# Kernel optimization log

Hardware: AMD Instinct MI355X
Metric: run time of the kernel (lower is better)

The kernel has to match this reference:

```python
import jax, jax.numpy as jnp
import numpy as np
from jax import lax

SEQ_LEN = 64
BATCH = 256
NUM_TAG = 32
EMBED = 256
HIDDEN = 256


def gru_cell(x, h, W_ih, W_hh, b_ih, b_hh):
    # PyTorch GRU cell: gates ordered (r, z, n)
    gi = x @ W_ih.T + b_ih
    gh = h @ W_hh.T + b_hh
    ir, iz, i_n = jnp.split(gi, 3, axis=-1)
    hr, hz, h_n = jnp.split(gh, 3, axis=-1)
    r = jax.nn.sigmoid(ir + hr)
    z = jax.nn.sigmoid(iz + hz)
    n = jnp.tanh(i_n + r * h_n)
    return (1.0 - z) * n + z * h


def setup_inputs() -> dict:
    key = jax.random.key(0)
    ks = jax.random.split(key, 9)
    emissions = jax.random.normal(ks[0], (SEQ_LEN, BATCH, NUM_TAG), jnp.float32)
    tags = jax.random.randint(ks[1], (SEQ_LEN, BATCH), 0, NUM_TAG)
    mask = jnp.ones((SEQ_LEN, BATCH), jnp.float32)
    s = float(1.0 / np.sqrt(HIDDEN))
    embedding = jax.random.normal(ks[2], (NUM_TAG + 1, EMBED), jnp.float32) * 0.1
    W_ih = jax.random.normal(ks[3], (3 * HIDDEN, EMBED), jnp.float32) * s
    W_hh = jax.random.normal(ks[4], (3 * HIDDEN, HIDDEN), jnp.float32) * s
    b_ih = jax.random.normal(ks[5], (3 * HIDDEN,), jnp.float32) * s
    b_hh = jax.random.normal(ks[6], (3 * HIDDEN,), jnp.float32) * s
    W_lin = jax.random.normal(ks[7], (NUM_TAG, HIDDEN), jnp.float32) * s
    b_lin = jnp.zeros((NUM_TAG,), jnp.float32)
    return {"emissions": emissions, "tags": tags, "mask": mask,
            "embedding": embedding, "W_ih": W_ih, "W_hh": W_hh,
            "b_ih": b_ih, "b_hh": b_hh, "W_lin": W_lin, "b_lin": b_lin}


def reference(emissions, tags, mask, embedding, W_ih, W_hh, b_ih, b_hh, W_lin, b_lin):
    L, B, T = emissions.shape
    H = W_hh.shape[1]
    K = T  # self.topk = num_tag in the original module
    mask = mask.astype(emissions.dtype)
    gru = lambda x, h: gru_cell(x, h, W_ih, W_hh, b_ih, b_hh)
    lin = lambda h: h @ W_lin.T + b_lin

    # shared initial step with start symbol y0 = num_tag
    x0 = jnp.broadcast_to(embedding[T], (B, embedding.shape[1]))
    h0 = jnp.zeros((B, H), emissions.dtype)
    h1 = gru(x0, h0)                      # (B,H)
    trans0 = lin(h1)                      # (B,T)
    em0 = emissions[0]
    bidx = jnp.arange(B)

    # ---- path score (faithful: emissions[0] gathered at EVERY timestep) ----
    t0 = tags[0]
    ps0 = (trans0[bidx, t0] + em0[bidx, t0]) * mask[0]

    def ps_step(carry, xs):
        h, s = carry
        pre, cur, m = xs
        h = gru(embedding[pre], h)
        tr = lin(h)
        s = s + (tr[bidx, cur] + em0[bidx, cur]) * m
        return (h, s), None

    (_, path_score), _ = lax.scan(ps_step, (h1, ps0), (tags[:-1], tags[1:], mask[1:]))

    # ---- approximate log-partition via beam search with K = num_tag beams ----
    s_init = (trans0 + em0) * mask[0][:, None]
    scores, beam_tags = lax.top_k(s_init, K)          # (B,K), tag-id indices
    hidden = jnp.broadcast_to(h1[:, None, :], (B, K, H))

    def lp_step(carry, xs):
        scores, beam_tags, hidden = carry
        em_t, m_t = xs
        x = embedding[beam_tags]                                  # (B,K,E)
        hnew = gru(x.reshape(B * K, -1), hidden.reshape(B * K, H)).reshape(B, K, H)
        tr = lin(hnew)                                            # (B,K,T)
        # faithful quirk: prior beam scores gathered by previous TAG id (K == T)
        base = jnp.take_along_axis(scores, beam_tags, axis=1)[:, :, None]
        cand = base + (tr + em_t[:, None, :]) * m_t[:, None, None]  # (B,K,T)
        new_scores, idx = lax.top_k(cand.reshape(B, K * T), K)
        new_tags = idx % T
        parent = idx // T
        new_hidden = jnp.take_along_axis(hnew, parent[:, :, None], axis=1)
        return (new_scores, new_tags, new_hidden), None

    (scores, _, _), _ = lax.scan(lp_step, (scores, beam_tags, hidden),
                                 (emissions[1:], mask[1:]))

    log_z = jax.nn.logsumexp(scores, axis=1)
    return (path_score - log_z).sum()
```

## Files before the change

### kernel.cpp

```cpp
#include <hip/hip_runtime.h>

#define SEQ 64
#define BAT 256
#define NT 32
#define EMB 256
#define HID 256
#define G3 768

typedef __bf16 bf16x8 __attribute__((ext_vector_type(8)));
typedef __bf16 bf16x4 __attribute__((ext_vector_type(4)));
typedef float f32x4 __attribute__((ext_vector_type(4)));
typedef unsigned long long ulx2 __attribute__((ext_vector_type(2)));

#define GL2S 265
#define HQS  280

__device__ __forceinline__ float sigm_fast(float x) {
    return __builtin_amdgcn_rcpf(1.f + __expf(-x));
}
__device__ __forceinline__ float tanh_fast(float x) {
    return 1.f - 2.f * __builtin_amdgcn_rcpf(__expf(2.f * x) + 1.f);
}
__device__ __forceinline__ float sigm(float x) {
    x = fminf(fmaxf(x, -30.f), 30.f);
    return 1.f / (1.f + __expf(-x));
}
__device__ __forceinline__ float tanhr(float x) {
    x = fminf(fmaxf(x, -15.f), 15.f);
    float e = __expf(2.f * x);
    return (e - 1.f) / (e + 1.f);
}

__global__ void k_pre(const float* __restrict__ emb, const float* __restrict__ W_ih,
                      const float* __restrict__ b_ih, const float* __restrict__ W_hh,
                      const float* __restrict__ W_lin, const float* __restrict__ b_hh,
                      const float* __restrict__ b_lin,
                      float* __restrict__ G, int2* __restrict__ Wpk8, __bf16* __restrict__ Wlpk,
                      float* __restrict__ h1, float* __restrict__ tr0)
{
    const int tid = threadIdx.x;
    const int blk = blockIdx.x;
    if (blk < 33) {
        __shared__ float es[EMB];
        __shared__ float hs[HID];
        es[tid] = emb[blk * EMB + tid];
        __syncthreads();
        const float4* e4 = (const float4*)es;
        float gv[3];
        #pragma unroll
        for (int g = 0; g < 3; ++g) {
            int c = g * HID + tid;
            const float4* w4 = (const float4*)(W_ih + c * EMB);
            float acc = b_ih[c];
            #pragma unroll 8
            for (int i = 0; i < EMB / 4; ++i) {
                float4 a = e4[i], w = w4[i];
                acc += a.x * w.x + a.y * w.y + a.z * w.z + a.w * w.w;
            }
            G[blk * G3 + c] = acc;
            gv[g] = acc;
        }
        if (blk == 32) {
            float r = sigm(gv[0] + b_hh[tid]);
            float z = sigm(gv[1] + b_hh[HID + tid]);
            float n = tanhr(gv[2] + r * b_hh[2 * HID + tid]);
            float h = (1.f - z) * n;
            h1[tid] = h; hs[tid] = h;
            __syncthreads();
            if (tid < NT) {
                const float4* w4 = (const float4*)(W_lin + tid * HID);
                const float4* h4 = (const float4*)hs;
                float acc = b_lin[tid];
                #pragma unroll 8
                for (int i = 0; i < HID / 4; ++i) {
                    float4 a = h4[i], w = w4[i];
                    acc += a.x * w.x + a.y * w.y + a.z * w.z + a.w * w.w;
                }
                tr0[tid] = acc;
            }
        }
    } else if (blk < 129) {
        int idx  = (blk - 33) * 256 + tid;
        int c    = idx >> 9;
        int rem  = idx & 511;
        int kt   = rem >> 6;
        int lane = rem & 63;
        int row  = c * 16 + (lane & 15);
        int col  = kt * 32 + (lane >> 4) * 8;
        const float* src = W_hh + row * 256 + col;
        int lo = __builtin_amdgcn_cvt_pk_fp8_f32(src[0], src[1], 0, 0);
        lo     = __builtin_amdgcn_cvt_pk_fp8_f32(src[2], src[3], lo, 1);
        int hi = __builtin_amdgcn_cvt_pk_fp8_f32(src[4], src[5], 0, 0);
        hi     = __builtin_amdgcn_cvt_pk_fp8_f32(src[6], src[7], hi, 1);
        Wpk8[idx] = make_int2(lo, hi);
    } else {
        int i2   = (blk - 129) * 256 + tid;
        int nt   = i2 >> 9;
        int rem  = i2 & 511;
        int kt   = rem >> 6;
        int lane = rem & 63;
        int row  = nt * 16 + (lane & 15);
        int col  = kt * 32 + (lane >> 4) * 8;
        const float* src = W_lin + row * 256 + col;
        bf16x8 v;
        #pragma unroll
        for (int j = 0; j < 8; ++j) v[j] = (__bf16)src[j];
        *(bf16x8*)(Wlpk + i2 * 8) = v;
    }
}

#define CLEANK32(mk, l32)                                          \
    _Pragma("unroll")                                              \
    for (int off_ = 16; off_ >= 1; off_ >>= 1) {                   \
        unsigned long long o_ = __shfl_xor((mk), off_, 64);        \
        bool up_ = ((l32) & off_) == 0;                            \
        if (up_ == (o_ > (mk))) (mk) = o_;                         \
    }

__global__ __launch_bounds__(1024, 1) void k_main(
    const float* __restrict__ em, const int* __restrict__ tags, const float* __restrict__ mask,
    const float* __restrict__ G, const float* __restrict__ h1w, const float* __restrict__ tr0w,
    const long* __restrict__ Wpk8, const __bf16* __restrict__ Wlpk,
    const float* __restrict__ bhhg, const float* __restrict__ bling,
    float* __restrict__ out)
{
    __shared__ __attribute__((aligned(16))) __bf16 gl2[33 * GL2S * 4];
    __shared__ __attribute__((aligned(16))) __bf16 hbuf[2][33 * 264];
    __shared__ __attribute__((aligned(16))) unsigned char hqb[2][33 * HQS];
    __shared__ __attribute__((aligned(16))) __bf16 wlin[8192];
    __shared__ __attribute__((aligned(16))) unsigned long long candk[32 * 34];
    __shared__ __attribute__((aligned(16))) unsigned long long srtk[16 * 33];
    __shared__ float trs32[33];
    __shared__ float em_s[SEQ * NT];
    __shared__ float mask_s[SEQ];
    __shared__ int tags_s[SEQ];
    __shared__ float scores[NT];
    __shared__ int par[NT];
    __shared__ int parbt[NT];
    __shared__ float s_ps;

    const int tid = threadIdx.x;
    const int b = blockIdx.x;
    const int w = tid >> 6;
    const int lane = tid & 63;
    const int q = lane >> 4;
    const int l15 = lane & 15;
    const int j = w * 16 + l15;

    long wreg[24];
    #pragma unroll
    for (int g = 0; g < 3; ++g)
        #pragma unroll
        for (int kt = 0; kt < 8; ++kt)
            wreg[g * 8 + kt] = Wpk8[((g * 16 + w) * 8 + kt) * 64 + lane];
    const float br_ = bhhg[j], bz_ = bhhg[256 + j], bn_ = bhhg[512 + j];
    float bl_ = 0.f;
    if (w < 6) bl_ = bling[(w & 1) * 16 + l15];

    if (tid < 64) mask_s[tid] = mask[tid * BAT + b];
    else if (tid < 128) tags_s[tid - 64] = tags[(tid - 64) * BAT + b];
    else if (tid < 160) par[tid - 128] = tid - 128;
    ((bf16x8*)wlin)[tid] = ((const bf16x8*)Wlpk)[tid];
    for (int idx = tid; idx < SEQ * NT; idx += 1024)
        em_s[idx] = em[((idx >> 5) * BAT + b) * NT + (idx & 31)];
    for (int idx = tid; idx < 33 * 256; idx += 1024) {
        int row = idx >> 8, j2 = idx & 255;
        const float* gp = G + row * 768 + j2;
        bf16x4 gv;
        gv[0] = (__bf16)gp[0]; gv[1] = (__bf16)gp[256];
        gv[2] = (__bf16)gp[512]; gv[3] = (__bf16)0.f;
        *(bf16x4*)&gl2[(row * GL2S + j2) * 4] = gv;
        hbuf[0][row * 264 + j2] = (__bf16)h1w[j2];
    }
    __syncthreads();
    for (int idx = tid; idx < 33 * 32; idx += 1024) {
        int row = idx >> 5, off = (idx & 31) * 8;
        bf16x8 hv = *(const bf16x8*)&hbuf[0][row * 264 + off];
        int lo = __builtin_amdgcn_cvt_pk_fp8_f32((float)hv[0], (float)hv[1], 0, 0);
        lo     = __builtin_amdgcn_cvt_pk_fp8_f32((float)hv[2], (float)hv[3], lo, 1);
        int hi = __builtin_amdgcn_cvt_pk_fp8_f32((float)hv[4], (float)hv[5], 0, 0);
        hi     = __builtin_amdgcn_cvt_pk_fp8_f32((float)hv[6], (float)hv[7], hi, 1);
        *(int2*)&hqb[0][row * HQS + off] = make_int2(lo, hi);
    }
    if (tid < 32) {
        float m0 = mask_s[0];
        float v = (tr0w[tid] + em_s[tid]) * m0;
        int cnt = 0;
        for (int jj = 0; jj < 32; ++jj) {
            float vj = __shfl(v, jj, 32);
            cnt += (vj > v) || (vj == v && jj < tid);
        }
        scores[cnt] = v;
        parbt[cnt] = (cnt << 8) | tid;
    }
    if (tid == 64) {
        int t0 = tags_s[0];
        s_ps = (tr0w[t0] + em_s[t0]) * mask_s[0];
    }
    __syncthreads();

    #pragma unroll 1
    for (int t = 1; t < SEQ; ++t) {
        const int cur = (t - 1) & 1, nxt = t & 1;
        const float m_t = mask_s[t];

        const int p0 = par[l15], p1 = par[16 + l15];
        const unsigned char* hqc = &hqb[cur][0];
        f32x4 acc[3][3];
        #pragma unroll
        for (int mt = 0; mt < 3; ++mt)
            #pragma unroll
            for (int g = 0; g < 3; ++g) {
                f32x4 z = {0.f, 0.f, 0.f, 0.f};
                acc[mt][g] = z;
            }
        #pragma unroll
        for (int kt = 0; kt < 8; ++kt) {
            const int kb = kt * 32 + q * 8;
            long af0 = *(const long*)(hqc + p0 * HQS + kb);
            long af1 = *(const long*)(hqc + p1 * HQS + kb);
            long a32 = *(const long*)(hqc + 32 * HQS + kb);
            long af2 = (l15 == 0) ? a32 : 0L;
            #pragma unroll
            for (int g = 0; g < 3; ++g) {
                acc[0][g] = __builtin_amdgcn_mfma_f32_16x16x32_fp8_fp8(af0, wreg[g * 8 + kt], acc[0][g], 0, 0, 0);
                acc[1][g] = __builtin_amdgcn_mfma_f32_16x16x32_fp8_fp8(af1, wreg[g * 8 + kt], acc[1][g], 0, 0, 0);
                acc[2][g] = __builtin_amdgcn_mfma_f32_16x16x32_fp8_fp8(af2, wreg[g * 8 + kt], acc[2][g], 0, 0, 0);
            }
        }

        {
            const int pt = tags_s[t - 1];
            #pragma unroll
            for (int mt = 0; mt < 2; ++mt) {
                #pragma unroll
                for (int r = 0; r < 4; ++r) {
                    const int row = mt * 16 + q * 4 + r;
                    const int pb = parbt[row];
                    const int e = pb & 255, src = pb >> 8;
                    bf16x4 g4 = *(const bf16x4*)&gl2[(e * GL2S + j) * 4];
                    float rr = sigm_fast((float)g4[0] + acc[mt][0][r] + br_);
                    float zz = sigm_fast((float)g4[1] + acc[mt][1][r] + bz_);
                    float nn = tanh_fast((float)g4[2] + rr * (acc[mt][2][r] + bn_));
                    float hold = (float)hbuf[cur][src * 264 + j];
                    hbuf[nxt][row * 264 + j] = (__bf16)(zz * (hold - nn) + nn);
                }
            }
            if (lane < 16) {
                bf16x4 g4 = *(const bf16x4*)&gl2[(pt * GL2S + j) * 4];
                float rr = sigm_fast((float)g4[0] + acc[2][0][0] + br_);
                float zz = sigm_fast((float)g4[1] + acc[2][1][0] + bz_);
                float nn = tanh_fast((float)g4[2] + rr * (acc[2][2][0] + bn_));
                float hold = (float)hbuf[cur][32 * 264 + j];
                hbuf[nxt][32 * 264 + j] = (__bf16)(zz * (hold - nn) + nn);
            }
        }
        __syncthreads();

        if (w < 6) {
            const int mt = w >> 1, ntc = w & 1;
            f32x4 a2 = {0.f, 0.f, 0.f, 0.f};
            #pragma unroll
            for (int kt = 0; kt < 8; ++kt) {
                const int kk = kt * 32 + q * 8;
                bf16x8 af;
                if (mt < 2) {
                    af = *(const bf16x8*)&hbuf[nxt][(mt * 16 + l15) * 264 + kk];
                } else {
                    bf16x8 rv = *(const bf16x8*)&hbuf[nxt][32 * 264 + kk];
                    bf16x8 z8 = (__bf16)0.f;
                    af = (l15 == 0) ? rv : z8;
                }
                bf16x8 bv = *(const bf16x8*)&wlin[((ntc * 8 + kt) * 64 + lane) * 8];
                a2 = __builtin_amdgcn_mfma_f32_16x16x32_bf16(af, bv, a2, 0, 0, 0);
            }
            const int colc = ntc * 16 + l15;
            if (mt < 2) {
                const float em_v = em_s[t * 32 + colc];
                #pragma unroll
                for (int r = 0; r < 4; ++r) {
                    const int row = mt * 16 + q * 4 + r;
                    float tr = a2[r] + bl_;
                    float bse = scores[parbt[row] & 255];
                    float v = bse + (tr + em_v) * m_t;
                    unsigned int vb = __float_as_uint(v);
                    unsigned int ov = vb ^ (0x80000000u | (unsigned int)(((int)vb) >> 31));
                    unsigned long long key =
                        ((unsigned long long)ov << 11) | (unsigned int)(1055 - (row * 32 + colc));
                    candk[row * 34 + colc] = key;
                }
            } else if (q == 0) {
                trs32[colc] = a2[0] + bl_;
            }
        } else {
            for (int c2 = tid - 384; c2 < 33 * 32; c2 += 640) {
                int row = c2 >> 5, off = (c2 & 31) * 8;
                bf16x8 hv = *(const bf16x8*)&hbuf[nxt][row * 264 + off];
                int lo = __builtin_amdgcn_cvt_pk_fp8_f32((float)hv[0], (float)hv[1], 0, 0);
                lo     = __builtin_amdgcn_cvt_pk_fp8_f32((float)hv[2], (float)hv[3], lo, 1);
                int hi = __builtin_amdgcn_cvt_pk_fp8_f32((float)hv[4], (float)hv[5], 0, 0);
                hi     = __builtin_amdgcn_cvt_pk_fp8_f32((float)hv[6], (float)hv[7], hi, 1);
                *(int2*)&hqb[nxt][row * HQS + off] = make_int2(lo, hi);
            }
        }
        __syncthreads();

        if (tid == 0) {
            int ct = tags_s[t];
            s_ps += (trs32[ct] + em_s[t * 32 + ct]) * m_t;
        }
        {
            const int half = lane >> 5, l32 = lane & 31;
            const int myrow = 2 * w + half;
            const unsigned long long own = candk[myrow * 34 + l32];
            const ulx2* pA = (const ulx2*)&candk[(2 * w) * 34];
            const ulx2* pB = (const ulx2*)&candk[(2 * w + 1) * 34];
            int cnt = 0;
            #pragma unroll
            for (int c = 0; c < 16; ++c) {
                ulx2 ka = pA[c];
                ulx2 kb2 = pB[c];
                cnt += (int)(ka[0] > own) + (int)(ka[1] > own)
                     + (int)(kb2[0] > own) + (int)(kb2[1] > own);
            }
            if (cnt < 32) srtk[w * 33 + cnt] = own;
        }
        __syncthreads();

        if (w < 4) {
            const int half = lane >> 5, l32 = lane & 31;
            const int rA = 4 * w + 2 * half, rB = rA + 1;
            unsigned long long a = srtk[rA * 33 + l32];
            unsigned long long bb = srtk[rB * 33 + (31 - l32)];
            unsigned long long m = (a > bb) ? a : bb;
            CLEANK32(m, l32);
            unsigned long long p = __shfl_xor(m, 63, 64);
            unsigned long long m2 = (m > p) ? m : p;
            CLEANK32(m2, l32);
            if (half == 0) srtk[(4 * w) * 33 + l32] = m2;
        }
        __syncthreads();

        if (w == 0) {
            const int half = lane >> 5, l32 = lane & 31;
            const int rA = 8 * half, rB = 8 * half + 4;
            unsigned long long a = srtk[rA * 33 + l32];
            unsigned long long bb = srtk[rB * 33 + (31 - l32)];
            unsigned long long m = (a > bb) ? a : bb;
            CLEANK32(m, l32);
            unsigned long long p = __shfl_xor(m, 63, 64);
            unsigned long long fv = (m > p) ? m : p;
            CLEANK32(fv, l32);
            if (half == 0) {
                unsigned int ov = (unsigned int)(fv >> 11);
                unsigned int bits = (ov & 0x80000000u) ? (ov ^ 0x80000000u) : ~ov;
                scores[l32] = __uint_as_float(bits);
                int fidx = 1055 - (int)(fv & 2047ULL);
                int pr = fidx >> 5, tg = fidx & 31;
                par[l32] = pr;
                parbt[l32] = (pr << 8) | tg;
            }
        }
        __syncthreads();
    }

    if (tid < 32) {
        float mx = scores[0];
        float ex = __expf(scores[tid] - mx);
        #pragma unroll
        for (int off = 16; off >= 1; off >>= 1) ex += __shfl_xor(ex, off, 32);
        if (tid == 0) {
            float logz = mx + logf(ex);
            atomicAdd(out, s_ps - logz);
        }
    }
}

extern "C" void kernel_launch(void* const* d_in, const int* in_sizes, int n_in,
                              void* d_out, int out_size, void* d_ws, size_t ws_size,
                              hipStream_t stream) {
    const float* emissions = (const float*)d_in[0];
    const int*   tags      = (const int*)d_in[1];
    const float* mask      = (const float*)d_in[2];
    const float* embedding = (const float*)d_in[3];
    const float* W_ih      = (const float*)d_in[4];
    const float* W_hh      = (const float*)d_in[5];
    const float* b_ih      = (const float*)d_in[6];
    const float* b_hh      = (const float*)d_in[7];
    const float* W_lin     = (const float*)d_in[8];
    const float* b_lin     = (const float*)d_in[9];
    float* out = (float*)d_out;

    char* ws = (char*)d_ws;
    float*  G    = (float*)ws;
    float*  h1   = (float*)(ws + 101376);
    float*  tr0  = (float*)(ws + 102400);
    int2*   Wpk8 = (int2*)(ws + 102528);
    __bf16* Wlpk = (__bf16*)(ws + 299136);

    hipMemsetAsync(d_out, 0, sizeof(float) * out_size, stream);
    k_pre<<<133, 256, 0, stream>>>(embedding, W_ih, b_ih, W_hh, W_lin, b_hh, b_lin,
                                   G, Wpk8, Wlpk, h1, tr0);
    k_main<<<BAT, 1024, 0, stream>>>(emissions, tags, mask, G, h1, tr0,
                                     (const long*)Wpk8, Wlpk, b_hh, b_lin, out);
}
```

Baseline: 653.1 us.

## Swap MFMA operands so each lane owns four hidden columns and fuse fp8 requantization

The GRU MFMA now takes the weights as the A operand and the hidden state as the B operand. This transposes the accumulator layout, so each lane holds four consecutive hidden units for one beam row. The gate epilogue then does vectorized bf16x4 loads and stores of the old and new hidden state, and it writes the fp8-packed hidden copy directly. That removes the separate requantization loop that waves 6-15 ran between barriers. The cost is more per-lane gather loads of gl2 (four rows per lane) and a different LDS access pattern that may cause bank conflicts.

Result: slower. 671.9 us (+2.9%).

```diff
diff --git a/kernel.cpp b/kernel.cpp
--- a/kernel.cpp
+++ b/kernel.cpp
@@ -14,6 +14,7 @@
 
 #define GL2S 265
 #define HQS  280
+#define HBS  264
 
 __device__ __forceinline__ float sigm_fast(float x) {
     return __builtin_amdgcn_rcpf(1.f + __expf(-x));
@@ -125,7 +126,7 @@
     float* __restrict__ out)
 {
     __shared__ __attribute__((aligned(16))) __bf16 gl2[33 * GL2S * 4];
-    __shared__ __attribute__((aligned(16))) __bf16 hbuf[2][33 * 264];
+    __shared__ __attribute__((aligned(16))) __bf16 hbuf[2][33 * HBS];
     __shared__ __attribute__((aligned(16))) unsigned char hqb[2][33 * HQS];
     __shared__ __attribute__((aligned(16))) __bf16 wlin[8192];
     __shared__ __attribute__((aligned(16))) unsigned long long candk[32 * 34];
@@ -145,7 +146,7 @@
     const int lane = tid & 63;
     const int q = lane >> 4;
     const int l15 = lane & 15;
-    const int j = w * 16 + l15;
+    const int j0 = w * 16 + q * 4;
 
     long wreg[24];
     #pragma unroll
@@ -153,7 +154,9 @@
         #pragma unroll
         for (int kt = 0; kt < 8; ++kt)
             wreg[g * 8 + kt] = Wpk8[((g * 16 + w) * 8 + kt) * 64 + lane];
-    const float br_ = bhhg[j], bz_ = bhhg[256 + j], bn_ = bhhg[512 + j];
+    const f32x4 br4 = *(const f32x4*)&bhhg[j0];
+    const f32x4 bz4 = *(const f32x4*)&bhhg[256 + j0];
+    const f32x4 bn4 = *(const f32x4*)&bhhg[512 + j0];
     float bl_ = 0.f;
     if (w < 6) bl_ = bling[(w & 1) * 16 + l15];
 
@@ -170,12 +173,12 @@
         gv[0] = (__bf16)gp[0]; gv[1] = (__bf16)gp[256];
         gv[2] = (__bf16)gp[512]; gv[3] = (__bf16)0.f;
         *(bf16x4*)&gl2[(row * GL2S + j2) * 4] = gv;
-        hbuf[0][row * 264 + j2] = (__bf16)h1w[j2];
+        hbuf[0][row * HBS + j2] = (__bf16)h1w[j2];
     }
     __syncthreads();
     for (int idx = tid; idx < 33 * 32; idx += 1024) {
         int row = idx >> 5, off = (idx & 31) * 8;
-        bf16x8 hv = *(const bf16x8*)&hbuf[0][row * 264 + off];
+        bf16x8 hv = *(const bf16x8*)&hbuf[0][row * HBS + off];
         int lo = __builtin_amdgcn_cvt_pk_fp8_f32((float)hv[0], (float)hv[1], 0, 0);
         lo     = __builtin_amdgcn_cvt_pk_fp8_f32((float)hv[2], (float)hv[3], lo, 1);
         int hi = __builtin_amdgcn_cvt_pk_fp8_f32((float)hv[4], (float)hv[5], 0, 0);
@@ -208,11 +211,11 @@
         const unsigned char* hqc = &hqb[cur][0];
         f32x4 acc[3][3];
         #pragma unroll
-        for (int mt = 0; mt < 3; ++mt)
+        for (int g = 0; g < 3; ++g)
             #pragma unroll
-            for (int g = 0; g < 3; ++g) {
+            for (int m = 0; m < 3; ++m) {
                 f32x4 z = {0.f, 0.f, 0.f, 0.f};
-                acc[mt][g] = z;
+                acc[g][m] = z;
             }
         #pragma unroll
         for (int kt = 0; kt < 8; ++kt) {
@@ -223,36 +226,51 @@
             long af2 = (l15 == 0) ? a32 : 0L;
             #pragma unroll
             for (int g = 0; g < 3; ++g) {
-                acc[0][g] = __builtin_amdgcn_mfma_f32_16x16x32_fp8_fp8(af0, wreg[g * 8 + kt], acc[0][g], 0, 0, 0);
-                acc[1][g] = __builtin_amdgcn_mfma_f32_16x16x32_fp8_fp8(af1, wreg[g * 8 + kt], acc[1][g], 0, 0, 0);
-                acc[2][g] = __builtin_amdgcn_mfma_f32_16x16x32_fp8_fp8(af2, wreg[g * 8 + kt], acc[2][g], 0, 0, 0);
+                acc[g][0] = __builtin_amdgcn_mfma_f32_16x16x32_fp8_fp8(wreg[g * 8 + kt], af0, acc[g][0], 0, 0, 0);
+                acc[g][1] = __builtin_amdgcn_mfma_f32_16x16x32_fp8_fp8(wreg[g * 8 + kt], af1, acc[g][1], 0, 0, 0);
+                acc[g][2] = __builtin_amdgcn_mfma_f32_16x16x32_fp8_fp8(wreg[g * 8 + kt], af2, acc[g][2], 0, 0, 0);
             }
         }
 
         {
             const int pt = tags_s[t - 1];
             #pragma unroll
-            for (int mt = 0; mt < 2; ++mt) {
+            for (int m = 0; m < 2; ++m) {
+                const int k = m * 16 + l15;
+                const int pb = parbt[k];
+                const int e = pb & 255, src = pb >> 8;
+                bf16x4 hold4 = *(const bf16x4*)&hbuf[cur][src * HBS + j0];
+                bf16x4 hv;
                 #pragma unroll
                 for (int r = 0; r < 4; ++r) {
-                    const int row = mt * 16 + q * 4 + r;
-                    const int pb = parbt[row];
-                    const int e = pb & 255, src = pb >> 8;
-                    bf16x4 g4 = *(const bf16x4*)&gl2[(e * GL2S + j) * 4];
-                    float rr = sigm_fast((float)g4[0] + acc[mt][0][r] + br_);
-                    float zz = sigm_fast((float)g4[1] + acc[mt][1][r] + bz_);
-                    float nn = tanh_fast((float)g4[2] + rr * (acc[mt][2][r] + bn_));
-                    float hold = (float)hbuf[cur][src * 264 + j];
-                    hbuf[nxt][row * 264 + j] = (__bf16)(zz * (hold - nn) + nn);
+                    bf16x4 g4 = *(const bf16x4*)&gl2[(e * GL2S + j0 + r) * 4];
+                    float rr = sigm_fast((float)g4[0] + acc[0][m][r] + br4[r]);
+                    float zz = sigm_fast((float)g4[1] + acc[1][m][r] + bz4[r]);
+                    float nn = tanh_fast((float)g4[2] + rr * (acc[2][m][r] + bn4[r]));
+                    float hold = (float)hold4[r];
+                    hv[r] = (__bf16)(zz * (hold - nn) + nn);
                 }
-            }
-            if (lane < 16) {
-                bf16x4 g4 = *(const bf16x4*)&gl2[(pt * GL2S + j) * 4];
-                float rr = sigm_fast((float)g4[0] + acc[2][0][0] + br_);
-                float zz = sigm_fast((float)g4[1] + acc[2][1][0] + bz_);
-                float nn = tanh_fast((float)g4[2] + rr * (acc[2][2][0] + bn_));
-                float hold = (float)hbuf[cur][32 * 264 + j];
-                hbuf[nxt][32 * 264 + j] = (__bf16)(zz * (hold - nn) + nn);
+                int pk = __builtin_amdgcn_cvt_pk_fp8_f32((float)hv[0], (float)hv[1], 0, 0);
+                pk     = __builtin_amdgcn_cvt_pk_fp8_f32((float)hv[2], (float)hv[3], pk, 1);
+                *(bf16x4*)&hbuf[nxt][k * HBS + j0] = hv;
+                *(int*)&hqb[nxt][k * HQS + j0] = pk;
+            }
+            if (l15 == 0) {
+                bf16x4 hold4 = *(const bf16x4*)&hbuf[cur][32 * HBS + j0];
+                bf16x4 hv;
+                #pragma unroll
+                for (int r = 0; r < 4; ++r) {
+                    bf16x4 g4 = *(const bf16x4*)&gl2[(pt * GL2S + j0 + r) * 4];
+                    float rr = sigm_fast((float)g4[0] + acc[0][2][r] + br4[r]);
+                    float zz = sigm_fast((float)g4[1] + acc[1][2][r] + bz4[r]);
+                    float nn = tanh_fast((float)g4[2] + rr * (acc[2][2][r] + bn4[r]));
+                    float hold = (float)hold4[r];
+                    hv[r] = (__bf16)(zz * (hold - nn) + nn);
+                }
+                int pk = __builtin_amdgcn_cvt_pk_fp8_f32((float)hv[0], (float)hv[1], 0, 0);
+                pk     = __builtin_amdgcn_cvt_pk_fp8_f32((float)hv[2], (float)hv[3], pk, 1);
+                *(bf16x4*)&hbuf[nxt][32 * HBS + j0] = hv;
+                *(int*)&hqb[nxt][32 * HQS + j0] = pk;
             }
         }
         __syncthreads();
@@ -265,9 +283,9 @@
                 const int kk = kt * 32 + q * 8;
                 bf16x8 af;
                 if (mt < 2) {
-                    af = *(const bf16x8*)&hbuf[nxt][(mt * 16 + l15) * 264 + kk];
+                    af = *(const bf16x8*)&hbuf[nxt][(mt * 16 + l15) * HBS + kk];
                 } else {
-                    bf16x8 rv = *(const bf16x8*)&hbuf[nxt][32 * 264 + kk];
+                    bf16x8 rv = *(const bf16x8*)&hbuf[nxt][32 * HBS + kk];
                     bf16x8 z8 = (__bf16)0.f;
                     af = (l15 == 0) ? rv : z8;
                 }
@@ -291,16 +309,6 @@
                 }
             } else if (q == 0) {
                 trs32[colc] = a2[0] + bl_;
-            }
-        } else {
-            for (int c2 = tid - 384; c2 < 33 * 32; c2 += 640) {
-                int row = c2 >> 5, off = (c2 & 31) * 8;
-                bf16x8 hv = *(const bf16x8*)&hbuf[nxt][row * 264 + off];
-                int lo = __builtin_amdgcn_cvt_pk_fp8_f32((float)hv[0], (float)hv[1], 0, 0);
-                lo     = __builtin_amdgcn_cvt_pk_fp8_f32((float)hv[2], (float)hv[3], lo, 1);
-                int hi = __builtin_amdgcn_cvt_pk_fp8_f32((float)hv[4], (float)hv[5], 0, 0);
-                hi     = __builtin_amdgcn_cvt_pk_fp8_f32((float)hv[6], (float)hv[7], hi, 1);
-                *(int2*)&hqb[nxt][row * HQS + off] = make_int2(lo, hi);
             }
         }
         __syncthreads();
```

## Precompute path-row GRU matmul during top-k merge and move fp8 requantization later

Applied to the files above, without the earlier changes.

Moves the fp8 quantization of the new hidden state from the candidate-scoring phase into the top-k merge phase, where warps 4+ are otherwise idle. Computes the gold-path row's recurrent MFMA (row 32) in the previous step's final phase, overlapping with warp 0's final merge. This drops one of the three MFMA row tiles from the critical per-step GRU matmul. In exchange it adds register pressure from the pacc accumulators, and the quantization now lands on a shorter phase with fewer threads available.

Result: faster. 580.1 us (-11.2%).

```diff
diff --git a/kernel.cpp b/kernel.cpp
--- a/kernel.cpp
+++ b/kernel.cpp
@@ -199,6 +199,20 @@
     }
     __syncthreads();
 
+    f32x4 pacc[3];
+    {
+        const unsigned char* hp = &hqb[0][32 * HQS];
+        #pragma unroll
+        for (int g = 0; g < 3; ++g) { f32x4 z = {0.f, 0.f, 0.f, 0.f}; pacc[g] = z; }
+        #pragma unroll
+        for (int kt = 0; kt < 8; ++kt) {
+            long a32 = *(const long*)(hp + kt * 32 + q * 8);
+            #pragma unroll
+            for (int g = 0; g < 3; ++g)
+                pacc[g] = __builtin_amdgcn_mfma_f32_16x16x32_fp8_fp8(a32, wreg[g * 8 + kt], pacc[g], 0, 0, 0);
+        }
+    }
+
     #pragma unroll 1
     for (int t = 1; t < SEQ; ++t) {
         const int cur = (t - 1) & 1, nxt = t & 1;
@@ -206,9 +220,9 @@
 
         const int p0 = par[l15], p1 = par[16 + l15];
         const unsigned char* hqc = &hqb[cur][0];
-        f32x4 acc[3][3];
-        #pragma unroll
-        for (int mt = 0; mt < 3; ++mt)
+        f32x4 acc[2][3];
+        #pragma unroll
+        for (int mt = 0; mt < 2; ++mt)
             #pragma unroll
             for (int g = 0; g < 3; ++g) {
                 f32x4 z = {0.f, 0.f, 0.f, 0.f};
@@ -219,13 +233,10 @@
             const int kb = kt * 32 + q * 8;
             long af0 = *(const long*)(hqc + p0 * HQS + kb);
             long af1 = *(const long*)(hqc + p1 * HQS + kb);
-            long a32 = *(const long*)(hqc + 32 * HQS + kb);
-            long af2 = (l15 == 0) ? a32 : 0L;
             #pragma unroll
             for (int g = 0; g < 3; ++g) {
                 acc[0][g] = __builtin_amdgcn_mfma_f32_16x16x32_fp8_fp8(af0, wreg[g * 8 + kt], acc[0][g], 0, 0, 0);
                 acc[1][g] = __builtin_amdgcn_mfma_f32_16x16x32_fp8_fp8(af1, wreg[g * 8 + kt], acc[1][g], 0, 0, 0);
-                acc[2][g] = __builtin_amdgcn_mfma_f32_16x16x32_fp8_fp8(af2, wreg[g * 8 + kt], acc[2][g], 0, 0, 0);
             }
         }
 
@@ -248,9 +259,9 @@
             }
             if (lane < 16) {
                 bf16x4 g4 = *(const bf16x4*)&gl2[(pt * GL2S + j) * 4];
-                float rr = sigm_fast((float)g4[0] + acc[2][0][0] + br_);
-                float zz = sigm_fast((float)g4[1] + acc[2][1][0] + bz_);
-                float nn = tanh_fast((float)g4[2] + rr * (acc[2][2][0] + bn_));
+                float rr = sigm_fast((float)g4[0] + pacc[0][0] + br_);
+                float zz = sigm_fast((float)g4[1] + pacc[1][0] + bz_);
+                float nn = tanh_fast((float)g4[2] + rr * (pacc[2][0] + bn_));
                 float hold = (float)hbuf[cur][32 * 264 + j];
                 hbuf[nxt][32 * 264 + j] = (__bf16)(zz * (hold - nn) + nn);
             }
@@ -292,16 +303,6 @@
             } else if (q == 0) {
                 trs32[colc] = a2[0] + bl_;
             }
-        } else {
-            for (int c2 = tid - 384; c2 < 33 * 32; c2 += 640) {
-                int row = c2 >> 5, off = (c2 & 31) * 8;
-                bf16x8 hv = *(const bf16x8*)&hbuf[nxt][row * 264 + off];
-                int lo = __builtin_amdgcn_cvt_pk_fp8_f32((float)hv[0], (float)hv[1], 0, 0);
-                lo     = __builtin_amdgcn_cvt_pk_fp8_f32((float)hv[2], (float)hv[3], lo, 1);
-                int hi = __builtin_amdgcn_cvt_pk_fp8_f32((float)hv[4], (float)hv[5], 0, 0);
-                hi     = __builtin_amdgcn_cvt_pk_fp8_f32((float)hv[6], (float)hv[7], hi, 1);
-                *(int2*)&hqb[nxt][row * HQS + off] = make_int2(lo, hi);
-            }
         }
         __syncthreads();
 
@@ -338,6 +339,16 @@
             unsigned long long m2 = (m > p) ? m : p;
             CLEANK32(m2, l32);
             if (half == 0) srtk[(4 * w) * 33 + l32] = m2;
+        } else {
+            for (int c2 = tid - 256; c2 < 33 * 32; c2 += 768) {
+                int row = c2 >> 5, off = (c2 & 31) * 8;
+                bf16x8 hv = *(const bf16x8*)&hbuf[nxt][row * 264 + off];
+                int lo = __builtin_amdgcn_cvt_pk_fp8_f32((float)hv[0], (float)hv[1], 0, 0);
+                lo     = __builtin_amdgcn_cvt_pk_fp8_f32((float)hv[2], (float)hv[3], lo, 1);
+                int hi = __builtin_amdgcn_cvt_pk_fp8_f32((float)hv[4], (float)hv[5], 0, 0);
+                hi     = __builtin_amdgcn_cvt_pk_fp8_f32((float)hv[6], (float)hv[7], hi, 1);
+                *(int2*)&hqb[nxt][row * HQS + off] = make_int2(lo, hi);
+            }
         }
         __syncthreads();
 
@@ -361,6 +372,18 @@
                 parbt[l32] = (pr << 8) | tg;
             }
         }
+        {
+            const unsigned char* hp = &hqb[nxt][32 * HQS];
+            #pragma unroll
+            for (int g = 0; g < 3; ++g) { f32x4 z = {0.f, 0.f, 0.f, 0.f}; pacc[g] = z; }
+            #pragma unroll
+            for (int kt = 0; kt < 8; ++kt) {
+                long a32 = *(const long*)(hp + kt * 32 + q * 8);
+                #pragma unroll
+                for (int g = 0; g < 3; ++g)
+                    pacc[g] = __builtin_amdgcn_mfma_f32_16x16x32_fp8_fp8(a32, wreg[g * 8 + kt], pacc[g], 0, 0, 0);
+            }
+        }
         __syncthreads();
     }
 
```
